# Performance work log

Hardware: AMD Instinct MI355X
Metric: run time of the kernel (lower is better)

The kernel has to match this reference:

```python
import jax, jax.numpy as jnp
jax.config.update("jax_enable_x64", True)
import numpy as np

B, S, D, H = 2, 1024, 1024, 16
DEPTH = D // H  # 64


def setup_inputs() -> dict:
    key = jax.random.key(0)
    ks = jax.random.split(key, 12)
    inp = {
        "q": jax.random.normal(ks[0], (B, S, D), jnp.float32),
        "k": jax.random.normal(ks[1], (B, S, D), jnp.float32),
        "v": jax.random.normal(ks[2], (B, S - 1, D), jnp.float32),
        "e": jnp.zeros((1,), jnp.float32),  # unused by the layer
        "mask": jax.random.randint(ks[3], (B, S - 1, S - 1), 0, 2, jnp.int32),
        "Wq": jax.random.normal(ks[4], (D, D), jnp.float32) * 0.02,
        "bq": jnp.zeros((D,), jnp.float32),
        "Wk": jax.random.normal(ks[5], (D, D), jnp.float32) * 0.02,
        "bk": jnp.zeros((D,), jnp.float32),
        "Wv": jax.random.normal(ks[6], (D, D), jnp.float32) * 0.02,
        "bv": jnp.zeros((D,), jnp.float32),
        "Wo": jax.random.normal(ks[7], (D, D), jnp.float32) * 0.02,
        "bo": jnp.zeros((D,), jnp.float32),
    }
    return inp


def _split_heads(x, b):
    # [b, s, D] -> [b, H, s, DEPTH]
    return x.reshape(b, -1, H, DEPTH).transpose(0, 2, 1, 3)


def reference(q, k, v, e, mask, Wq, bq, Wk, bk, Wv, bv, Wo, bo):
    b = q.shape[0]
    qh = _split_heads(q @ Wq + bq, b)  # [b,H,S,dh]
    kh = _split_heads(k @ Wk + bk, b)  # [b,H,S,dh]
    vh = _split_heads(v @ Wv + bv, b)  # [b,H,S-1,dh]
    # QK^T then asymmetric offset slice [1:, :-1]
    scores = jnp.einsum("bhqd,bhkd->bhqk", qh, kh)[:, :, 1:, :-1]  # [b,H,S-1,S-1]
    inv_sqrt_dk = 1.0 / jnp.sqrt(jnp.float32(DEPTH))
    nl_qk = jax.nn.relu(scores * inv_sqrt_dk).astype(jnp.float64)
    nl_qk = nl_qk + mask[:, None, :, :].astype(jnp.float64) * (-1e9)
    att_weights = jax.nn.softmax(nl_qk, axis=-1)  # fp64, [b,H,S-1,S-1]
    out = jnp.einsum("bhqk,bhkd->bhqd", att_weights, vh.astype(jnp.float64))
    out = out.transpose(0, 2, 1, 3).reshape(b, -1, H * DEPTH)  # [b,S-1,D]
    output = out.astype(jnp.float32) @ Wo + bo
    return (output, att_weights)
```

## Files before the change

### kernel.cpp

```cpp
#include <hip/hip_runtime.h>
#include <math.h>

#define HN 16
#define SEQ 1024
#define DMODEL 1024
#define DH 64
#define SM1 1023

typedef float  f32x4  __attribute__((ext_vector_type(4)));
typedef __bf16 bf16x8 __attribute__((ext_vector_type(8)));

#define ROWB 272
#define VROWB 560

template<int MODE>
__global__ __launch_bounds__(256)
void gemm_mfma_kernel(const float* __restrict__ X, const float* __restrict__ W,
                      const float* __restrict__ bias, float* __restrict__ out32,
                      __bf16* __restrict__ outHi, __bf16* __restrict__ outLo,
                      int M, int rows)
{
    __shared__ __align__(16) __bf16 As[4096];
    __shared__ __align__(16) __bf16 Bs[4096];

    const int t  = threadIdx.x;
    const int w  = t >> 6, l = t & 63;
    const int lr = l & 15, ls = l >> 4;
    const int m0 = blockIdx.y * 64, n0 = blockIdx.x * 64;
    const int sr  = t >> 2;
    const int skq = t & 3;

    f32x4 acc[4];
#pragma unroll
    for (int ct = 0; ct < 4; ++ct) acc[ct] = f32x4{0.f, 0.f, 0.f, 0.f};

    const int ar   = w * 16 + lr;
    const int a_hi = ar * 128 + (((2 * ls    ) ^ (ar & 7)) << 4);
    const int a_lo = ar * 128 + (((2 * ls + 1) ^ (ar & 7)) << 4);
    const int st_hi = sr * 128 + (((2 * skq    ) ^ (sr & 7)) << 4);
    const int st_lo = sr * 128 + (((2 * skq + 1) ^ (sr & 7)) << 4);

    for (int k0 = 0; k0 < DMODEL; k0 += 32) {
        __syncthreads();
        {
            float xv[8];
            if (m0 + sr < M) {
                float4 v0 = *(const float4*)&X[(size_t)(m0 + sr) * DMODEL + k0 + skq * 8];
                float4 v1 = *(const float4*)&X[(size_t)(m0 + sr) * DMODEL + k0 + skq * 8 + 4];
                xv[0] = v0.x; xv[1] = v0.y; xv[2] = v0.z; xv[3] = v0.w;
                xv[4] = v1.x; xv[5] = v1.y; xv[6] = v1.z; xv[7] = v1.w;
            } else {
#pragma unroll
                for (int e = 0; e < 8; ++e) xv[e] = 0.f;
            }
            bf16x8 h8, l8;
#pragma unroll
            for (int e = 0; e < 8; ++e) {
                __bf16 hb = (__bf16)xv[e];
                h8[e] = hb;
                l8[e] = (__bf16)(xv[e] - (float)hb);
            }
            *(bf16x8*)((char*)As + st_hi) = h8;
            *(bf16x8*)((char*)As + st_lo) = l8;
        }
        {
            float wv[8];
#pragma unroll
            for (int e = 0; e < 8; ++e)
                wv[e] = W[(size_t)(k0 + skq * 8 + e) * DMODEL + n0 + sr];
            bf16x8 h8, l8;
#pragma unroll
            for (int e = 0; e < 8; ++e) {
                __bf16 hb = (__bf16)wv[e];
                h8[e] = hb;
                l8[e] = (__bf16)(wv[e] - (float)hb);
            }
            *(bf16x8*)((char*)Bs + st_hi) = h8;
            *(bf16x8*)((char*)Bs + st_lo) = l8;
        }
        __syncthreads();

        const bf16x8 ah = *(const bf16x8*)((const char*)As + a_hi);
        const bf16x8 al = *(const bf16x8*)((const char*)As + a_lo);
#pragma unroll
        for (int ct = 0; ct < 4; ++ct) {
            const int bc   = ct * 16 + lr;
            const int b_hi = bc * 128 + (((2 * ls    ) ^ (bc & 7)) << 4);
            const int b_lo = bc * 128 + (((2 * ls + 1) ^ (bc & 7)) << 4);
            const bf16x8 bh = *(const bf16x8*)((const char*)Bs + b_hi);
            const bf16x8 bl = *(const bf16x8*)((const char*)Bs + b_lo);
            acc[ct] = __builtin_amdgcn_mfma_f32_16x16x32_bf16(ah, bh, acc[ct], 0, 0, 0);
            acc[ct] = __builtin_amdgcn_mfma_f32_16x16x32_bf16(al, bh, acc[ct], 0, 0, 0);
            acc[ct] = __builtin_amdgcn_mfma_f32_16x16x32_bf16(ah, bl, acc[ct], 0, 0, 0);
        }
    }

#pragma unroll
    for (int ct = 0; ct < 4; ++ct) {
        const int n = n0 + ct * 16 + lr;
        const float bv = bias[n];
#pragma unroll
        for (int j = 0; j < 4; ++j) {
            const int m = m0 + w * 16 + ls * 4 + j;
            if (m >= M) continue;
            const float val = acc[ct][j] + bv;
            if (MODE == 1) {
                out32[(size_t)m * DMODEL + n] = val;
            } else {
                const int bb = m / rows, s = m - bb * rows;
                const __bf16 hb = (__bf16)val;
                const __bf16 lb = (__bf16)(val - (float)hb);
                size_t idx;
                if (MODE == 0)
                    idx = (((size_t)(bb * HN + (n >> 6)) * SEQ + s) << 6) + (n & 63);
                else
                    idx = (((size_t)(bb * HN + (n >> 6)) * DH + (n & 63)) << 10) + s;
                outHi[idx] = hb; outLo[idx] = lb;
            }
        }
    }
}

__global__ __launch_bounds__(256)
void mask_pack_kernel(const int* __restrict__ mask, unsigned int* __restrict__ mb)
{
    const int row = blockIdx.x * 4 + (threadIdx.x >> 6);
    const int l   = threadIdx.x & 63;
    if (row >= 2 * SM1) return;
    const int* mrow = mask + (size_t)row * SM1;
    unsigned int* out = mb + (size_t)row * 32;
#pragma unroll
    for (int i = 0; i < 16; ++i) {
        const int c = i * 64 + l;
        const bool mv = (c < SM1) && (mrow[c] != 0);
        unsigned long long bal = __ballot(mv);
        if (l == 0) {
            out[i * 2]     = (unsigned int)bal;
            out[i * 2 + 1] = (unsigned int)(bal >> 32);
        }
    }
}

__global__ __launch_bounds__(512)
void attn_fused_kernel(const __bf16* __restrict__ qhi, const __bf16* __restrict__ qlo,
                       const __bf16* __restrict__ khi, const __bf16* __restrict__ klo,
                       const __bf16* __restrict__ vthi, const __bf16* __restrict__ vtlo,
                       const unsigned int* __restrict__ mbG,
                       float* __restrict__ att, float* __restrict__ ctx)
{
    __shared__ __align__(16) char Qs[64 * ROWB];
    __shared__ __align__(16) char KV[35840];
    __shared__ __align__(16) float E[64 * 132];
    __shared__ float invs[64];
    __shared__ float partial[64][2];
    __shared__ unsigned int mbits[64][4];

    const int b = blockIdx.z, h = blockIdx.y, bh = b * HN + h;
    const int q0 = blockIdx.x * 64;
    const int t = threadIdx.x, w = t >> 6, l = t & 63;
    const int lr = l & 15, ls = l >> 4;
    const int g = w & 3, p = w >> 2;

#pragma unroll
    for (int it = 0; it < 2; ++it) {
        const int id = t + it * 512;
        const int r = id >> 4, cw = id & 15;
        const int plane = cw >> 3, s = cw & 7;
        int qrow = q0 + r + 1; if (qrow > 1023) qrow = 1023;
        const __bf16* src = plane ? qlo : qhi;
        bf16x8 vv = *(const bf16x8*)&src[((size_t)bh * SEQ + qrow) * DH + s * 8];
        *(bf16x8*)(Qs + r * ROWB + cw * 16) = vv;
    }
    __syncthreads();

    const int ar = g * 16 + lr;
    const bf16x8 a0h = *(const bf16x8*)(Qs + ar * ROWB + ls * 16);
    const bf16x8 a1h = *(const bf16x8*)(Qs + ar * ROWB + (4 + ls) * 16);
    const bf16x8 a0l = *(const bf16x8*)(Qs + ar * ROWB + (8 + ls) * 16);
    const bf16x8 a1l = *(const bf16x8*)(Qs + ar * ROWB + (12 + ls) * 16);

    float rsum[4] = {0.f, 0.f, 0.f, 0.f};
    for (int kt = 0; kt < 8; ++kt) {
        const int c0 = kt * 128;
        __syncthreads();
        if (t < 256) {
            const int r = t >> 2, wd = t & 3;
            const int rr = q0 + r;
            mbits[r][wd] = (rr < SM1) ? mbG[((size_t)b * SM1 + rr) * 32 + kt * 4 + wd] : 0u;
        }
#pragma unroll
        for (int it = 0; it < 4; ++it) {
            const int id = t + it * 512;
            const int r = id >> 4, cw = id & 15;
            const int plane = cw >> 3, s = cw & 7;
            int krow = c0 + r; if (krow > 1023) krow = 1023;
            const __bf16* src = plane ? klo : khi;
            bf16x8 vv = *(const bf16x8*)&src[((size_t)bh * SEQ + krow) * DH + s * 8];
            *(bf16x8*)(KV + r * ROWB + cw * 16) = vv;
        }
        __syncthreads();

#pragma unroll
        for (int i = 0; i < 4; ++i) {
            const int ct = p * 4 + i;
            const int kr = ct * 16 + lr;
            const bf16x8 b0h = *(const bf16x8*)(KV + kr * ROWB + ls * 16);
            const bf16x8 b1h = *(const bf16x8*)(KV + kr * ROWB + (4 + ls) * 16);
            const bf16x8 b0l = *(const bf16x8*)(KV + kr * ROWB + (8 + ls) * 16);
            const bf16x8 b1l = *(const bf16x8*)(KV + kr * ROWB + (12 + ls) * 16);

            f32x4 acc = {0.f, 0.f, 0.f, 0.f};
            acc = __builtin_amdgcn_mfma_f32_16x16x32_bf16(a0h, b0h, acc, 0, 0, 0);
            acc = __builtin_amdgcn_mfma_f32_16x16x32_bf16(a0l, b0h, acc, 0, 0, 0);
            acc = __builtin_amdgcn_mfma_f32_16x16x32_bf16(a0h, b0l, acc, 0, 0, 0);
            acc = __builtin_amdgcn_mfma_f32_16x16x32_bf16(a1h, b1h, acc, 0, 0, 0);
            acc = __builtin_amdgcn_mfma_f32_16x16x32_bf16(a1l, b1h, acc, 0, 0, 0);
            acc = __builtin_amdgcn_mfma_f32_16x16x32_bf16(a1h, b1l, acc, 0, 0, 0);

            const int c = c0 + ct * 16 + lr;
#pragma unroll
            for (int j = 0; j < 4; ++j) {
                const int r = q0 + g * 16 + ls * 4 + j;
                if (r < SM1 && c < SM1) {
                    float sc = fmaxf(acc[j] * 0.125f, 0.f);
                    const unsigned int wm = mbits[g * 16 + ls * 4 + j][ct >> 1];
                    if ((wm >> ((ct & 1) * 16 + lr)) & 1u) sc = -1e9f;
                    rsum[j] += __expf(sc);
                }
            }
        }
    }
#pragma unroll
    for (int j = 0; j < 4; ++j) {
        rsum[j] += __shfl_xor(rsum[j], 1, 64);
        rsum[j] += __shfl_xor(rsum[j], 2, 64);
        rsum[j] += __shfl_xor(rsum[j], 4, 64);
        rsum[j] += __shfl_xor(rsum[j], 8, 64);
    }
    if (lr == 0) {
#pragma unroll
        for (int j = 0; j < 4; ++j)
            partial[g * 16 + ls * 4 + j][p] = rsum[j];
    }
    __syncthreads();
    if (t < 64) {
        const float s = partial[t][0] + partial[t][1];
        invs[t] = (q0 + t < SM1) ? 1.0f / s : 0.f;
    }
    __syncthreads();
    float inv4[4];
#pragma unroll
    for (int j = 0; j < 4; ++j) inv4[j] = invs[g * 16 + ls * 4 + j];

    f32x4 oacc[4];
#pragma unroll
    for (int ct = 0; ct < 4; ++ct) oacc[ct] = f32x4{0.f, 0.f, 0.f, 0.f};

    for (int kt = 0; kt < 8; ++kt) {
        const int c0 = kt * 128;
        __syncthreads();
        if (t < 256) {
            const int r = t >> 2, wd = t & 3;
            const int rr = q0 + r;
            mbits[r][wd] = (rr < SM1) ? mbG[((size_t)b * SM1 + rr) * 32 + kt * 4 + wd] : 0u;
        }
#pragma unroll
        for (int it = 0; it < 4; ++it) {
            const int id = t + it * 512;
            const int r = id >> 4, cw = id & 15;
            const int plane = cw >> 3, s = cw & 7;
            int krow = c0 + r; if (krow > 1023) krow = 1023;
            const __bf16* src = plane ? klo : khi;
            bf16x8 vv = *(const bf16x8*)&src[((size_t)bh * SEQ + krow) * DH + s * 8];
            *(bf16x8*)(KV + r * ROWB + cw * 16) = vv;
        }
        __syncthreads();

#pragma unroll
        for (int i = 0; i < 4; ++i) {
            const int ct = p * 4 + i;
            const int kr = ct * 16 + lr;
            const bf16x8 b0h = *(const bf16x8*)(KV + kr * ROWB + ls * 16);
            const bf16x8 b1h = *(const bf16x8*)(KV + kr * ROWB + (4 + ls) * 16);
            const bf16x8 b0l = *(const bf16x8*)(KV + kr * ROWB + (8 + ls) * 16);
            const bf16x8 b1l = *(const bf16x8*)(KV + kr * ROWB + (12 + ls) * 16);

            f32x4 acc = {0.f, 0.f, 0.f, 0.f};
            acc = __builtin_amdgcn_mfma_f32_16x16x32_bf16(a0h, b0h, acc, 0, 0, 0);
            acc = __builtin_amdgcn_mfma_f32_16x16x32_bf16(a0l, b0h, acc, 0, 0, 0);
            acc = __builtin_amdgcn_mfma_f32_16x16x32_bf16(a0h, b0l, acc, 0, 0, 0);
            acc = __builtin_amdgcn_mfma_f32_16x16x32_bf16(a1h, b1h, acc, 0, 0, 0);
            acc = __builtin_amdgcn_mfma_f32_16x16x32_bf16(a1l, b1h, acc, 0, 0, 0);
            acc = __builtin_amdgcn_mfma_f32_16x16x32_bf16(a1h, b1l, acc, 0, 0, 0);

            const int c = c0 + ct * 16 + lr;
#pragma unroll
            for (int j = 0; j < 4; ++j) {
                const int r = q0 + g * 16 + ls * 4 + j;
                float v = 0.f;
                if (r < SM1 && c < SM1) {
                    float sc = fmaxf(acc[j] * 0.125f, 0.f);
                    const unsigned int wm = mbits[g * 16 + ls * 4 + j][ct >> 1];
                    if ((wm >> ((ct & 1) * 16 + lr)) & 1u) sc = -1e9f;
                    v = __expf(sc) * inv4[j];
                }
                E[(g * 16 + ls * 4 + j) * 132 + ct * 16 + lr] = v;
            }
        }
        __syncthreads();

#pragma unroll
        for (int it = 0; it < 4; ++it) {
            const int id = t + it * 512;
            const int dr = id >> 5, cw = id & 31;
            const int plane = cw >> 4, s8 = cw & 15;
            const __bf16* src = plane ? vtlo : vthi;
            bf16x8 vv = *(const bf16x8*)&src[(((size_t)bh * DH + dr) << 10) + c0 + s8 * 8];
            *(bf16x8*)(KV + dr * VROWB + cw * 16) = vv;
        }
#pragma unroll
        for (int it = 0; it < 4; ++it) {
            const int id = t + it * 512;
            const int r = id >> 5, q4 = id & 31;
            const int rr = q0 + r, cc = c0 + q4 * 4;
            if (rr < SM1) {
                f32x4 vv = *(const f32x4*)&E[r * 132 + q4 * 4];
                float* dst = &att[((size_t)bh * SM1 + rr) * SM1 + cc];
                if (cc + 4 <= SM1) {
                    __builtin_nontemporal_store(vv, (f32x4*)dst);
                } else {
                    if (cc + 0 < SM1) dst[0] = vv.x;
                    if (cc + 1 < SM1) dst[1] = vv.y;
                    if (cc + 2 < SM1) dst[2] = vv.z;
                }
            }
        }
        __syncthreads();

#pragma unroll
        for (int m = 0; m < 2; ++m) {
            const int ks = p * 2 + m;
            const int pr = g * 16 + lr;
            const f32x4 p0 = *(const f32x4*)&E[pr * 132 + ks * 32 + ls * 8];
            const f32x4 p1 = *(const f32x4*)&E[pr * 132 + ks * 32 + ls * 8 + 4];
            float pf[8] = {p0.x, p0.y, p0.z, p0.w, p1.x, p1.y, p1.z, p1.w};
            bf16x8 ph, pl;
#pragma unroll
            for (int e = 0; e < 8; ++e) {
                const __bf16 hb = (__bf16)pf[e];
                ph[e] = hb;
                pl[e] = (__bf16)(pf[e] - (float)hb);
            }
#pragma unroll
            for (int ct = 0; ct < 4; ++ct) {
                const int vr = ct * 16 + lr;
                const bf16x8 vh = *(const bf16x8*)(KV + vr * VROWB + (ks * 4 + ls) * 16);
                const bf16x8 vl = *(const bf16x8*)(KV + vr * VROWB + (16 + ks * 4 + ls) * 16);
                oacc[ct] = __builtin_amdgcn_mfma_f32_16x16x32_bf16(ph, vh, oacc[ct], 0, 0, 0);
                oacc[ct] = __builtin_amdgcn_mfma_f32_16x16x32_bf16(pl, vh, oacc[ct], 0, 0, 0);
                oacc[ct] = __builtin_amdgcn_mfma_f32_16x16x32_bf16(ph, vl, oacc[ct], 0, 0, 0);
            }
        }
    }

    __syncthreads();
    float* red = (float*)Qs;
    if (p == 1) {
#pragma unroll
        for (int ct = 0; ct < 4; ++ct)
#pragma unroll
            for (int j = 0; j < 4; ++j)
                red[(g * 16 + ls * 4 + j) * 68 + ct * 16 + lr] = oacc[ct][j];
    }
    __syncthreads();
    if (p == 0) {
#pragma unroll
        for (int ct = 0; ct < 4; ++ct)
#pragma unroll
            for (int j = 0; j < 4; ++j) {
                const int r = q0 + g * 16 + ls * 4 + j;
                if (r < SM1)
                    ctx[((size_t)b * SM1 + r) * DMODEL + h * DH + ct * 16 + lr] =
                        oacc[ct][j] + red[(g * 16 + ls * 4 + j) * 68 + ct * 16 + lr];
            }
    }
}

extern "C" void kernel_launch(void* const* d_in, const int* in_sizes, int n_in,
                              void* d_out, int out_size, void* d_ws, size_t ws_size,
                              hipStream_t stream) {
    const float* q    = (const float*)d_in[0];
    const float* k    = (const float*)d_in[1];
    const float* v    = (const float*)d_in[2];
    const int*   mask = (const int*)  d_in[4];
    const float* Wq   = (const float*)d_in[5];
    const float* bq   = (const float*)d_in[6];
    const float* Wk   = (const float*)d_in[7];
    const float* bk   = (const float*)d_in[8];
    const float* Wv   = (const float*)d_in[9];
    const float* bv   = (const float*)d_in[10];
    const float* Wo   = (const float*)d_in[11];
    const float* bo   = (const float*)d_in[12];

    float* out0 = (float*)d_out;
    float* att  = out0 + (size_t)2 * SM1 * DMODEL;

    const size_t NQ  = (size_t)2 * HN * SEQ * DH;
    const size_t NVT = (size_t)2 * HN * DH * 1024;
    __bf16* ws16 = (__bf16*)d_ws;
    __bf16* qhi  = ws16;
    __bf16* qlo  = qhi + NQ;
    __bf16* khi  = qlo + NQ;
    __bf16* klo  = khi + NQ;
    __bf16* vthi = klo + NQ;
    __bf16* vtlo = vthi + NVT;
    float*  ctx  = (float*)(vtlo + NVT);
    unsigned int* mbG = (unsigned int*)(ctx + (size_t)2 * SM1 * DMODEL);

    (void)hipMemsetAsync(vthi, 0, 2 * NVT * sizeof(__bf16), stream);

    mask_pack_kernel<<<dim3(512), 256, 0, stream>>>(mask, mbG);

    gemm_mfma_kernel<0><<<dim3(16, 32), 256, 0, stream>>>(q, Wq, bq, nullptr, qhi, qlo, 2 * SEQ, SEQ);
    gemm_mfma_kernel<0><<<dim3(16, 32), 256, 0, stream>>>(k, Wk, bk, nullptr, khi, klo, 2 * SEQ, SEQ);
    gemm_mfma_kernel<2><<<dim3(16, 32), 256, 0, stream>>>(v, Wv, bv, nullptr, vthi, vtlo, 2 * SM1, SM1);

    attn_fused_kernel<<<dim3(16, HN, 2), 512, 0, stream>>>(qhi, qlo, khi, klo, vthi, vtlo, mbG, att, ctx);

    gemm_mfma_kernel<1><<<dim3(16, 32), 256, 0, stream>>>(ctx, Wo, bo, out0, nullptr, nullptr, 2 * SM1, SM1);
}
```

Baseline: 265.1 us.

## Shrink attention LDS with XOR swizzle, alias Q/E buffer, preload mask bits

Replaces the padded LDS rows (272/560-byte strides) with dense rows addressed through an XOR swizzle. The Q staging buffer is reused as the probability tile E, which cuts the shared-memory footprint and lets launch bounds ask for 4 blocks per CU. All 32 mask words per row are loaded once into a transposed table instead of being reloaded every key tile, and s_setprio is placed around the MFMA sequences. In exchange the kernel carries more register pressure under the tighter launch bound and needs an extra barrier after the Q fragments are read.

```diff
diff --git a/kernel.cpp b/kernel.cpp
--- a/kernel.cpp
+++ b/kernel.cpp
@@ -9,9 +9,6 @@
 
 typedef float  f32x4  __attribute__((ext_vector_type(4)));
 typedef __bf16 bf16x8 __attribute__((ext_vector_type(8)));
-
-#define ROWB 272
-#define VROWB 560
 
 template<int MODE>
 __global__ __launch_bounds__(256)
@@ -141,19 +138,18 @@
     }
 }
 
-__global__ __launch_bounds__(512)
+__global__ __launch_bounds__(512, 4)
 void attn_fused_kernel(const __bf16* __restrict__ qhi, const __bf16* __restrict__ qlo,
                        const __bf16* __restrict__ khi, const __bf16* __restrict__ klo,
                        const __bf16* __restrict__ vthi, const __bf16* __restrict__ vtlo,
                        const unsigned int* __restrict__ mbG,
                        float* __restrict__ att, float* __restrict__ ctx)
 {
-    __shared__ __align__(16) char Qs[64 * ROWB];
-    __shared__ __align__(16) char KV[35840];
-    __shared__ __align__(16) float E[64 * 132];
+    __shared__ __align__(16) char QE[64 * 528];
+    __shared__ __align__(16) char KV[32768];
+    __shared__ unsigned int mbitsT[32][64];
     __shared__ float invs[64];
     __shared__ float partial[64][2];
-    __shared__ unsigned int mbits[64][4];
 
     const int b = blockIdx.z, h = blockIdx.y, bh = b * HN + h;
     const int q0 = blockIdx.x * 64;
@@ -169,25 +165,28 @@
         int qrow = q0 + r + 1; if (qrow > 1023) qrow = 1023;
         const __bf16* src = plane ? qlo : qhi;
         bf16x8 vv = *(const bf16x8*)&src[((size_t)bh * SEQ + qrow) * DH + s * 8];
-        *(bf16x8*)(Qs + r * ROWB + cw * 16) = vv;
+        *(bf16x8*)(QE + r * 256 + ((cw ^ (r & 15)) << 4)) = vv;
+    }
+#pragma unroll
+    for (int it = 0; it < 4; ++it) {
+        const int id = t + it * 512;
+        const int cw = id & 31, r = id >> 5;
+        const int rr = q0 + r;
+        mbitsT[cw][r] = (rr < SM1) ? mbG[((size_t)b * SM1 + rr) * 32 + cw] : 0u;
     }
     __syncthreads();
 
     const int ar = g * 16 + lr;
-    const bf16x8 a0h = *(const bf16x8*)(Qs + ar * ROWB + ls * 16);
-    const bf16x8 a1h = *(const bf16x8*)(Qs + ar * ROWB + (4 + ls) * 16);
-    const bf16x8 a0l = *(const bf16x8*)(Qs + ar * ROWB + (8 + ls) * 16);
-    const bf16x8 a1l = *(const bf16x8*)(Qs + ar * ROWB + (12 + ls) * 16);
+    const bf16x8 a0h = *(const bf16x8*)(QE + ar * 256 + (((ls     ) ^ lr) << 4));
+    const bf16x8 a1h = *(const bf16x8*)(QE + ar * 256 + ((( 4 + ls) ^ lr) << 4));
+    const bf16x8 a0l = *(const bf16x8*)(QE + ar * 256 + ((( 8 + ls) ^ lr) << 4));
+    const bf16x8 a1l = *(const bf16x8*)(QE + ar * 256 + (((12 + ls) ^ lr) << 4));
+    __syncthreads();
 
     float rsum[4] = {0.f, 0.f, 0.f, 0.f};
     for (int kt = 0; kt < 8; ++kt) {
         const int c0 = kt * 128;
         __syncthreads();
-        if (t < 256) {
-            const int r = t >> 2, wd = t & 3;
-            const int rr = q0 + r;
-            mbits[r][wd] = (rr < SM1) ? mbG[((size_t)b * SM1 + rr) * 32 + kt * 4 + wd] : 0u;
-        }
 #pragma unroll
         for (int it = 0; it < 4; ++it) {
             const int id = t + it * 512;
@@ -196,7 +195,7 @@
             int krow = c0 + r; if (krow > 1023) krow = 1023;
             const __bf16* src = plane ? klo : khi;
             bf16x8 vv = *(const bf16x8*)&src[((size_t)bh * SEQ + krow) * DH + s * 8];
-            *(bf16x8*)(KV + r * ROWB + cw * 16) = vv;
+            *(bf16x8*)(KV + r * 256 + ((cw ^ (r & 15)) << 4)) = vv;
         }
         __syncthreads();
 
@@ -204,26 +203,29 @@
         for (int i = 0; i < 4; ++i) {
             const int ct = p * 4 + i;
             const int kr = ct * 16 + lr;
-            const bf16x8 b0h = *(const bf16x8*)(KV + kr * ROWB + ls * 16);
-            const bf16x8 b1h = *(const bf16x8*)(KV + kr * ROWB + (4 + ls) * 16);
-            const bf16x8 b0l = *(const bf16x8*)(KV + kr * ROWB + (8 + ls) * 16);
-            const bf16x8 b1l = *(const bf16x8*)(KV + kr * ROWB + (12 + ls) * 16);
+            const bf16x8 b0h = *(const bf16x8*)(KV + kr * 256 + (((ls     ) ^ lr) << 4));
+            const bf16x8 b1h = *(const bf16x8*)(KV + kr * 256 + ((( 4 + ls) ^ lr) << 4));
+            const bf16x8 b0l = *(const bf16x8*)(KV + kr * 256 + ((( 8 + ls) ^ lr) << 4));
+            const bf16x8 b1l = *(const bf16x8*)(KV + kr * 256 + (((12 + ls) ^ lr) << 4));
 
             f32x4 acc = {0.f, 0.f, 0.f, 0.f};
+            __builtin_amdgcn_s_setprio(1);
             acc = __builtin_amdgcn_mfma_f32_16x16x32_bf16(a0h, b0h, acc, 0, 0, 0);
             acc = __builtin_amdgcn_mfma_f32_16x16x32_bf16(a0l, b0h, acc, 0, 0, 0);
             acc = __builtin_amdgcn_mfma_f32_16x16x32_bf16(a0h, b0l, acc, 0, 0, 0);
             acc = __builtin_amdgcn_mfma_f32_16x16x32_bf16(a1h, b1h, acc, 0, 0, 0);
             acc = __builtin_amdgcn_mfma_f32_16x16x32_bf16(a1l, b1h, acc, 0, 0, 0);
             acc = __builtin_amdgcn_mfma_f32_16x16x32_bf16(a1h, b1l, acc, 0, 0, 0);
+            __builtin_amdgcn_s_setprio(0);
 
             const int c = c0 + ct * 16 + lr;
+            const int wmi = kt * 4 + (ct >> 1);
 #pragma unroll
             for (int j = 0; j < 4; ++j) {
                 const int r = q0 + g * 16 + ls * 4 + j;
                 if (r < SM1 && c < SM1) {
                     float sc = fmaxf(acc[j] * 0.125f, 0.f);
-                    const unsigned int wm = mbits[g * 16 + ls * 4 + j][ct >> 1];
+                    const unsigned int wm = mbitsT[wmi][g * 16 + ls * 4 + j];
                     if ((wm >> ((ct & 1) * 16 + lr)) & 1u) sc = -1e9f;
                     rsum[j] += __expf(sc);
                 }
@@ -252,6 +254,7 @@
 #pragma unroll
     for (int j = 0; j < 4; ++j) inv4[j] = invs[g * 16 + ls * 4 + j];
 
+    float* E = (float*)QE;
     f32x4 oacc[4];
 #pragma unroll
     for (int ct = 0; ct < 4; ++ct) oacc[ct] = f32x4{0.f, 0.f, 0.f, 0.f};
@@ -259,11 +262,6 @@
     for (int kt = 0; kt < 8; ++kt) {
         const int c0 = kt * 128;
         __syncthreads();
-        if (t < 256) {
-            const int r = t >> 2, wd = t & 3;
-            const int rr = q0 + r;
-            mbits[r][wd] = (rr < SM1) ? mbG[((size_t)b * SM1 + rr) * 32 + kt * 4 + wd] : 0u;
-        }
 #pragma unroll
         for (int it = 0; it < 4; ++it) {
             const int id = t + it * 512;
@@ -272,7 +270,7 @@
             int krow = c0 + r; if (krow > 1023) krow = 1023;
             const __bf16* src = plane ? klo : khi;
             bf16x8 vv = *(const bf16x8*)&src[((size_t)bh * SEQ + krow) * DH + s * 8];
-            *(bf16x8*)(KV + r * ROWB + cw * 16) = vv;
+            *(bf16x8*)(KV + r * 256 + ((cw ^ (r & 15)) << 4)) = vv;
         }
         __syncthreads();
 
@@ -280,27 +278,30 @@
         for (int i = 0; i < 4; ++i) {
             const int ct = p * 4 + i;
             const int kr = ct * 16 + lr;
-            const bf16x8 b0h = *(const bf16x8*)(KV + kr * ROWB + ls * 16);
-            const bf16x8 b1h = *(const bf16x8*)(KV + kr * ROWB + (4 + ls) * 16);
-            const bf16x8 b0l = *(const bf16x8*)(KV + kr * ROWB + (8 + ls) * 16);
-            const bf16x8 b1l = *(const bf16x8*)(KV + kr * ROWB + (12 + ls) * 16);
+            const bf16x8 b0h = *(const bf16x8*)(KV + kr * 256 + (((ls     ) ^ lr) << 4));
+            const bf16x8 b1h = *(const bf16x8*)(KV + kr * 256 + ((( 4 + ls) ^ lr) << 4));
+            const bf16x8 b0l = *(const bf16x8*)(KV + kr * 256 + ((( 8 + ls) ^ lr) << 4));
+            const bf16x8 b1l = *(const bf16x8*)(KV + kr * 256 + (((12 + ls) ^ lr) << 4));
 
             f32x4 acc = {0.f, 0.f, 0.f, 0.f};
+            __builtin_amdgcn_s_setprio(1);
             acc = __builtin_amdgcn_mfma_f32_16x16x32_bf16(a0h, b0h, acc, 0, 0, 0);
             acc = __builtin_amdgcn_mfma_f32_16x16x32_bf16(a0l, b0h, acc, 0, 0, 0);
             acc = __builtin_amdgcn_mfma_f32_16x16x32_bf16(a0h, b0l, acc, 0, 0, 0);
             acc = __builtin_amdgcn_mfma_f32_16x16x32_bf16(a1h, b1h, acc, 0, 0, 0);
             acc = __builtin_amdgcn_mfma_f32_16x16x32_bf16(a1l, b1h, acc, 0, 0, 0);
             acc = __builtin_amdgcn_mfma_f32_16x16x32_bf16(a1h, b1l, acc, 0, 0, 0);
+            __builtin_amdgcn_s_setprio(0);
 
             const int c = c0 + ct * 16 + lr;
+            const int wmi = kt * 4 + (ct >> 1);
 #pragma unroll
             for (int j = 0; j < 4; ++j) {
                 const int r = q0 + g * 16 + ls * 4 + j;
                 float v = 0.f;
                 if (r < SM1 && c < SM1) {
                     float sc = fmaxf(acc[j] * 0.125f, 0.f);
-                    const unsigned int wm = mbits[g * 16 + ls * 4 + j][ct >> 1];
+                    const unsigned int wm = mbitsT[wmi][g * 16 + ls * 4 + j];
                     if ((wm >> ((ct & 1) * 16 + lr)) & 1u) sc = -1e9f;
                     v = __expf(sc) * inv4[j];
                 }
@@ -316,7 +317,7 @@
             const int plane = cw >> 4, s8 = cw & 15;
             const __bf16* src = plane ? vtlo : vthi;
             bf16x8 vv = *(const bf16x8*)&src[(((size_t)bh * DH + dr) << 10) + c0 + s8 * 8];
-            *(bf16x8*)(KV + dr * VROWB + cw * 16) = vv;
+            *(bf16x8*)(KV + dr * 512 + ((cw ^ (dr & 31)) << 4)) = vv;
         }
 #pragma unroll
         for (int it = 0; it < 4; ++it) {
@@ -354,17 +355,21 @@
 #pragma unroll
             for (int ct = 0; ct < 4; ++ct) {
                 const int vr = ct * 16 + lr;
-                const bf16x8 vh = *(const bf16x8*)(KV + vr * VROWB + (ks * 4 + ls) * 16);
-                const bf16x8 vl = *(const bf16x8*)(KV + vr * VROWB + (16 + ks * 4 + ls) * 16);
+                const int hslot = ((ks * 4 + ls) ^ (vr & 31));
+                const int lslot = ((16 + ks * 4 + ls) ^ (vr & 31));
+                const bf16x8 vh = *(const bf16x8*)(KV + vr * 512 + (hslot << 4));
+                const bf16x8 vl = *(const bf16x8*)(KV + vr * 512 + (lslot << 4));
+                __builtin_amdgcn_s_setprio(1);
                 oacc[ct] = __builtin_amdgcn_mfma_f32_16x16x32_bf16(ph, vh, oacc[ct], 0, 0, 0);
                 oacc[ct] = __builtin_amdgcn_mfma_f32_16x16x32_bf16(pl, vh, oacc[ct], 0, 0, 0);
                 oacc[ct] = __builtin_amdgcn_mfma_f32_16x16x32_bf16(ph, vl, oacc[ct], 0, 0, 0);
-            }
-        }
-    }
-
-    __syncthreads();
-    float* red = (float*)Qs;
+                __builtin_amdgcn_s_setprio(0);
+            }
+        }
+    }
+
+    __syncthreads();
+    float* red = (float*)QE;
     if (p == 1) {
 #pragma unroll
         for (int ct = 0; ct < 4; ++ct)
```

Result: slower. 295.5 us (+11.5%).
